# Kernel tuning notes

Measured on AMD Instinct MI355X. Metric: run time of the kernel, lower is better.

The kernel has to match this reference:

```python
import jax, jax.numpy as jnp
import numpy as np

TOP_K = 2
NUM_EXPERTS = 8


def setup_inputs() -> dict:
    key = jax.random.key(0)
    ks = jax.random.split(key, 8)
    h, d, ds, E = 1024, 512, 1024, NUM_EXPERTS
    s = 1.0 / np.sqrt(h)
    return {
        "x": jax.random.normal(ks[0], (2, 2048, h), jnp.float32),
        "router": jax.random.normal(ks[1], (h, E), jnp.float32) * s,
        "experts_gate": jax.random.normal(ks[2], (E, h, d), jnp.float32) * s,
        "experts_up": jax.random.normal(ks[3], (E, h, d), jnp.float32) * s,
        "experts_down": jax.random.normal(ks[4], (E, d, h), jnp.float32) * (1.0 / np.sqrt(d)),
        "shared_gate": jax.random.normal(ks[5], (h, ds), jnp.float32) * s,
        "shared_up": jax.random.normal(ks[6], (h, ds), jnp.float32) * s,
        "shared_down": jax.random.normal(ks[7], (ds, h), jnp.float32) * (1.0 / np.sqrt(ds)),
    }


def reference(x, router, experts_gate, experts_up, experts_down,
              shared_gate, shared_up, shared_down):
    b, s, h = x.shape
    E = router.shape[1]
    # Shared expert path (SwiGLU)
    shared_act = jax.nn.silu(jnp.einsum('bsh,hd->bsd', x, shared_gate))
    shared_up_out = jnp.einsum('bsh,hd->bsd', x, shared_up)
    shared_out = jnp.einsum('bsd,dh->bsh', shared_act * shared_up_out, shared_down)
    # Router: softmax over experts, top-k selection
    router_probs = jax.nn.softmax(jnp.einsum('bsh,he->bse', x, router), axis=-1)
    topk_probs, topk_idx = jax.lax.top_k(router_probs, TOP_K)  # [b,s,k]
    # Dense per-token expert coefficient matrix: coef[t,e] = prob if expert e selected else 0
    coef = jnp.sum(jax.nn.one_hot(topk_idx, E, dtype=x.dtype) * topk_probs[..., None], axis=2)
    coef = coef.reshape(b * s, E)  # [T,E]
    x_flat = x.reshape(b * s, h)
    # Grouped expert SwiGLU (mathematically identical to gather->gemm->scatter_add;
    # unrouted token contributions are zeroed by coef)
    gate = jnp.einsum('th,ehd->etd', x_flat, experts_gate)
    up = jnp.einsum('th,ehd->etd', x_flat, experts_up)
    expert_out = jnp.einsum('etd,edh->eth', jax.nn.silu(gate) * up, experts_down)
    routed = jnp.einsum('eth,te->th', expert_out, coef)
    return routed.reshape(b, s, h) + shared_out
```

## Files before the change

kernel.cpp:

```cpp
#include <hip/hip_runtime.h>
#include <hip/hip_bf16.h>
#include <stdint.h>

typedef short bf16x8 __attribute__((ext_vector_type(8)));
typedef float f32x4 __attribute__((ext_vector_type(4)));
typedef unsigned short u16;

#define GLOAD16(gp, lp)                                                        \
  __builtin_amdgcn_global_load_lds(                                            \
      (const __attribute__((address_space(1))) void*)(gp),                     \
      (__attribute__((address_space(3))) void*)(lp), 16, 0, 0)

__device__ __forceinline__ u16 f2bf(float f) {
  uint32_t u = __builtin_bit_cast(uint32_t, f);
  u = (u + 0x7FFFu + ((u >> 16) & 1u)) >> 16;
  return (u16)u;
}
__device__ __forceinline__ float bf2f(u16 v) {
  return __builtin_bit_cast(float, (uint32_t)v << 16);
}

__device__ __forceinline__ int swzoff(int row, int u) {
  int p = row >> 1;
  int us = ((row & 1) * 4 + u) ^ (p & 7);
  return p * 128 + us * 16;
}

__global__ void mega(const float* __restrict__ x, const float* __restrict__ rw,
                     const float* __restrict__ eg, const float* __restrict__ eu,
                     const float* __restrict__ ed, const float* __restrict__ sg,
                     const float* __restrict__ su, const float* __restrict__ sd,
                     u16* __restrict__ Xb, u16* __restrict__ WpT,
                     u16* __restrict__ Wd2, u16* __restrict__ Wds,
                     float4* __restrict__ meta) {
  __shared__ float t[64][65];
  const int tid = threadIdx.x;
  const int b = blockIdx.x;
  if (b < 1280) {
    const float* src; int k0, h0;
    const bool is_e = b < 1024;
    if (is_e) { src = ed; k0 = (b >> 4) * 64;          h0 = (b & 15) * 64; }
    else      { src = sd; k0 = ((b - 1024) >> 4) * 64; h0 = (b & 15) * 64; }
#pragma unroll
    for (int p = 0; p < 4; ++p) {
      int r = p * 16 + (tid >> 4), c = (tid & 15) * 4;
      float4 v = *(const float4*)&src[(size_t)(k0 + r) * 1024 + h0 + c];
      t[r][c] = v.x; t[r][c + 1] = v.y; t[r][c + 2] = v.z; t[r][c + 3] = v.w;
    }
    __syncthreads();
#pragma unroll
    for (int p = 0; p < 4; ++p) {
      int hl = p * 16 + (tid >> 4), kl = (tid & 15) * 4;
      ushort4 o;
      o.x = f2bf(t[kl][hl]);     o.y = f2bf(t[kl + 1][hl]);
      o.z = f2bf(t[kl + 2][hl]); o.w = f2bf(t[kl + 3][hl]);
      if (is_e) {
        int kk = k0 + kl;
        int e = kk >> 9, dk = kk & 511;
        *(ushort4*)&Wd2[(size_t)e * 524288 + (size_t)(h0 + hl) * 512 + dk] = o;
      } else {
        *(ushort4*)&Wds[(size_t)(h0 + hl) * 1024 + k0 + kl] = o;
      }
    }
  } else if (b < 3840) {
    int bb = b - 1280;
    const float* src; int pbase, C, dt, ht;
    if (bb < 2048) {
      int slice = bb >> 7, r = bb & 127;
      int e = slice >> 1; int up = slice & 1;
      src = (up ? eu : eg) + (size_t)e * 524288;
      pbase = e * 1024 + up * 32; C = 512;
      dt = r >> 4; ht = r & 15;
    } else {
      int r = bb - 2048;
      int up = r >= 256; r &= 255;
      src = up ? su : sg; pbase = 8192 + up * 32; C = 1024;
      dt = r >> 4; ht = r & 15;
    }
    const int d0 = dt * 64, h0 = ht * 64;
#pragma unroll
    for (int p = 0; p < 4; ++p) {
      int hl = p * 16 + (tid >> 4), dl = (tid & 15) * 4;
      float4 v = *(const float4*)&src[(size_t)(h0 + hl) * C + d0 + dl];
      t[hl][dl] = v.x; t[hl][dl + 1] = v.y; t[hl][dl + 2] = v.z; t[hl][dl + 3] = v.w;
    }
    __syncthreads();
#pragma unroll
    for (int p = 0; p < 4; ++p) {
      int dl = p * 16 + (tid >> 4), hl = (tid & 15) * 4;
      int d = d0 + dl;
      int prow = pbase + ((d >> 5) << 6) + (d & 31);
      ushort4 o;
      o.x = f2bf(t[hl][dl]);     o.y = f2bf(t[hl + 1][dl]);
      o.z = f2bf(t[hl + 2][dl]); o.w = f2bf(t[hl + 3][dl]);
      *(ushort4*)&WpT[(size_t)prow * 1024 + h0 + hl] = o;
    }
  } else if (b < 4864) {
    const int l = tid & 63;
    const int tok = (b - 3840) * 4 + (tid >> 6);
    const float* xr = x + (size_t)tok * 1024;
    float acc[8];
#pragma unroll
    for (int e = 0; e < 8; ++e) acc[e] = 0.f;
    for (int it = 0; it < 16; ++it) {
      int h = it * 64 + l;
      float xv = xr[h];
      float4 r0 = *(const float4*)&rw[h * 8];
      float4 r1 = *(const float4*)&rw[h * 8 + 4];
      acc[0] += xv * r0.x; acc[1] += xv * r0.y; acc[2] += xv * r0.z; acc[3] += xv * r0.w;
      acc[4] += xv * r1.x; acc[5] += xv * r1.y; acc[6] += xv * r1.z; acc[7] += xv * r1.w;
    }
#pragma unroll
    for (int off = 32; off >= 1; off >>= 1) {
#pragma unroll
      for (int e = 0; e < 8; ++e) acc[e] += __shfl_xor(acc[e], off, 64);
    }
    if (l == 0) {
      float m = acc[0];
#pragma unroll
      for (int e = 1; e < 8; ++e) m = fmaxf(m, acc[e]);
      float p[8], s = 0.f;
#pragma unroll
      for (int e = 0; e < 8; ++e) { p[e] = expf(acc[e] - m); s += p[e]; }
      int i1 = 0;
#pragma unroll
      for (int e = 1; e < 8; ++e) if (p[e] > p[i1]) i1 = e;
      int i2 = (i1 == 0) ? 1 : 0;
#pragma unroll
      for (int e = 0; e < 8; ++e) if (e != i1 && p[e] > p[i2]) i2 = e;
      float inv = 1.f / s;
      meta[tok] = make_float4(__int_as_float(i1), __int_as_float(i2),
                              p[i1] * inv, p[i2] * inv);
    }
  } else {
    int i = (b - 4864) * 512 + tid;
#pragma unroll
    for (int k = 0; k < 2; ++k) {
      float4 v = ((const float4*)x)[i + k * 256];
      ushort4 o;
      o.x = f2bf(v.x); o.y = f2bf(v.y); o.z = f2bf(v.z); o.w = f2bf(v.w);
      ((ushort4*)Xb)[i + k * 256] = o;
    }
  }
}

__global__ __launch_bounds__(512) void assign_k(const float4* __restrict__ meta,
                                                int* __restrict__ counts_g,
                                                int* __restrict__ list_tok,
                                                int2* __restrict__ t2s) {
  __shared__ u16 sel[4096];
  __shared__ int cnt_s[8];
  const int tid = threadIdx.x;
  for (int i = tid; i < 4096; i += 512) {
    float4 m = meta[i];
    sel[i] = (u16)(__float_as_int(m.x) | (__float_as_int(m.y) << 8));
  }
  __syncthreads();

  const int E = tid >> 6;
  const int lane = tid & 63;
  const unsigned long long lt = (lane == 63) ? ~0ull >> 1 : ((1ull << lane) - 1ull);

  int total = 0;
#pragma unroll 8
  for (int it = 0; it < 64; ++it) {
    u16 s = sel[it * 64 + lane];
    bool any = ((s & 255) == E) || ((s >> 8) == E);
    total += __popcll(__ballot(any));
  }
  if (lane == 0) { cnt_s[E] = total; counts_g[E] = total; }
  __syncthreads();
  int base = 0;
#pragma unroll
  for (int e = 0; e < 8; ++e) base += (e < E) ? cnt_s[e] : 0;

  int running = base;
  for (int it = 0; it < 64; ++it) {
    int tok = it * 64 + lane;
    u16 s = sel[tok];
    bool s1 = ((s & 255) == E);
    bool s2 = ((s >> 8) == E);
    unsigned long long mask = __ballot(s1 || s2);
    int pos = running + __popcll(mask & lt);
    if (s1 || s2) {
      list_tok[pos] = tok;
      if (s1) t2s[tok].x = pos;
      else    t2s[tok].y = pos;
    }
    running += __popcll(mask);
  }
}

template <int MODE>
__global__ __launch_bounds__(512, 2) void moe_gemm(
    const u16* __restrict__ Xb, const u16* __restrict__ WpT,
    const u16* __restrict__ Wd2, const u16* __restrict__ Wds,
    u16* __restrict__ Hs, u16* __restrict__ Hcomp, u16* __restrict__ Pb,
    u16* __restrict__ Ps0, u16* __restrict__ Ps1,
    const int* __restrict__ counts, const int* __restrict__ list_tok) {
  constexpr int SLOT = (128 + 256) * 64;
  constexpr int BOFF = 128 * 64;
  __shared__ __align__(16) char lds[3 * SLOT];

  const int tid = threadIdx.x;
  const int l = tid & 63, l15 = l & 15, lg = l >> 4;
  const int wv = tid >> 6, wr = wv >> 2, wc = wv & 3;

  const int id = blockIdx.x;
  const bool routed = id < 288;
  int expert = 0, m0 = 0, n0 = 0, base = 0, count = 0, nt, split = 0, kb = 0;

  if (routed) {
    int mtf = id >> 2; n0 = (id & 3) * 256;
    int acc_ = 0, bas = 0, found = 0;
#pragma unroll
    for (int e = 0; e < 8; ++e) {
      int c = counts[e];
      int nm = (c + 127) >> 7;
      if (!found && mtf < acc_ + nm) {
        expert = e; m0 = (mtf - acc_) * 128; base = bas; count = c; found = 1;
      }
      acc_ += nm; bas += c;
    }
    if (!found) return;
  } else {
    int sid = id - 288;
    int xcd = sid & 7, pos = sid >> 3;
    int mG = xcd >> 1, nG = xcd & 1;
    if (MODE == 0) {
      int mL = pos & 7, nL = pos >> 3;
      m0 = (mG * 8 + mL) * 128; n0 = (nG * 4 + nL) * 256;
    } else {
      split = pos & 1;
      int q = pos >> 1;
      int mL = q & 7, nL = q >> 3;
      m0 = (mG * 8 + mL) * 128; n0 = (nG * 2 + nL) * 256;
      kb = split * 512;
    }
  }
  nt = (MODE == 1) ? 16 : 32;

  const char* gA0; const char* gB[2]; int lA0, lB[2];
  {
    int L = tid * 16;
    int p = L >> 7, uph = (L >> 4) & 7;
    int usw = uph ^ (p & 7);
    int row = 2 * p + (usw >> 2), ulog = usw & 3;
    const u16* ap;
    if (MODE == 0) {
      if (routed) {
        int ar = min(m0 + row, count - 1);
        ap = Xb + (size_t)list_tok[base + ar] * 1024;
      } else ap = Xb + (size_t)(m0 + row) * 1024;
    } else {
      if (routed) ap = Hcomp + (size_t)(base + min(m0 + row, count - 1)) * 512;
      else        ap = Hs + (size_t)(m0 + row) * 1024 + kb;
    }
    gA0 = (const char*)ap + ulog * 16;
    lA0 = L;
  }
#pragma unroll
  for (int j = 0; j < 2; ++j) {
    int L = (j * 512 + tid) * 16;
    int p = L >> 7, uph = (L >> 4) & 7;
    int usw = uph ^ (p & 7);
    int row = 2 * p + (usw >> 2), ulog = usw & 3;
    const u16* bp;
    if (MODE == 0) {
      int rbase = routed ? expert * 1024 : 8192;
      bp = WpT + (size_t)(rbase + n0 + row) * 1024;
    } else {
      if (routed) bp = Wd2 + (size_t)expert * 524288 + (size_t)(n0 + row) * 512;
      else        bp = Wds + (size_t)(n0 + row) * 1024 + kb;
    }
    gB[j] = (const char*)bp + ulog * 16;
    lB[j] = L;
  }

  int offA[4], offB[4];
#pragma unroll
  for (int m = 0; m < 4; ++m) offA[m] = swzoff(wr * 64 + m * 16 + l15, lg);
#pragma unroll
  for (int n = 0; n < 4; ++n) offB[n] = BOFF + swzoff(wc * 64 + n * 16 + l15, lg);

  f32x4 acc[4][4];
#pragma unroll
  for (int m = 0; m < 4; ++m)
#pragma unroll
    for (int n = 0; n < 4; ++n) acc[m][n] = {0.f, 0.f, 0.f, 0.f};

#define STAGE(T)                                                               \
  {                                                                            \
    char* sb_ = lds + (((T) % 3) * SLOT);                                      \
    const int tb_ = (T) * 64;                                                  \
    GLOAD16(gA0 + tb_, sb_ + lA0);                                             \
    GLOAD16(gB[0] + tb_, sb_ + BOFF + lB[0]);                                  \
    GLOAD16(gB[1] + tb_, sb_ + BOFF + lB[1]);                                  \
  }

  STAGE(0); STAGE(1);

  for (int t = 0; t < nt; ++t) {
    if (t + 1 < nt) {
      asm volatile("s_waitcnt vmcnt(3)" ::: "memory");
    } else {
      asm volatile("s_waitcnt vmcnt(0)" ::: "memory");
    }
    __builtin_amdgcn_s_barrier();
    asm volatile("" ::: "memory");
    char* sb = lds + ((t % 3) * SLOT);
    bf16x8 af[4], bfr[4];
#pragma unroll
    for (int m = 0; m < 4; ++m) af[m] = *(const bf16x8*)(sb + offA[m]);
#pragma unroll
    for (int n = 0; n < 4; ++n) bfr[n] = *(const bf16x8*)(sb + offB[n]);
    if (t + 2 < nt) STAGE(t + 2);
    __builtin_amdgcn_s_setprio(1);
#pragma unroll
    for (int m = 0; m < 4; ++m)
#pragma unroll
      for (int n = 0; n < 4; ++n)
        acc[m][n] = __builtin_amdgcn_mfma_f32_16x16x32_bf16(af[m], bfr[n], acc[m][n], 0, 0, 0);
    __builtin_amdgcn_s_setprio(0);
    asm volatile("" ::: "memory");
  }
#undef STAGE

  const int rbl = wr * 64 + lg * 4;
  const int cnt_lim = routed ? count : (1 << 30);
  if constexpr (MODE == 0) {
    u16* dst = routed ? Hcomp : Hs;
    const int ldH = routed ? 512 : 1024;
    const int rowbase = routed ? (base + m0) : m0;
    const int cD0 = (n0 + wc * 64) >> 1;
#pragma unroll
    for (int m = 0; m < 4; ++m)
#pragma unroll
      for (int q = 0; q < 2; ++q) {
        int cD = cD0 + q * 16 + l15;
#pragma unroll
        for (int j = 0; j < 4; ++j) {
          int mrow = rbl + m * 16 + j;
          if (m0 + mrow < cnt_lim) {
            float g = acc[m][q][j];
            float u = acc[m][q + 2][j];
            dst[(size_t)(rowbase + mrow) * ldH + cD] =
                f2bf(g / (1.f + __expf(-g)) * u);
          }
        }
      }
  } else {
    const int cb = n0 + wc * 64;
    u16* dstS = split ? Ps1 : Ps0;
#pragma unroll
    for (int m = 0; m < 4; ++m)
#pragma unroll
      for (int n = 0; n < 4; ++n)
#pragma unroll
        for (int j = 0; j < 4; ++j) {
          int mrow = rbl + m * 16 + j;
          if (m0 + mrow < cnt_lim) {
            int col = cb + n * 16 + l15;
            if (routed)
              Pb[(size_t)(base + m0 + mrow) * 1024 + col] = f2bf(acc[m][n][j]);
            else
              dstS[(size_t)(m0 + mrow) * 1024 + col] = f2bf(acc[m][n][j]);
          }
        }
  }
}

__global__ void reduce_k(const float4* __restrict__ meta, const int2* __restrict__ t2s,
                         const u16* __restrict__ Pb, const u16* __restrict__ Ps0,
                         const u16* __restrict__ Ps1, float* __restrict__ out) {
  const int t = blockIdx.x;
  const int c = threadIdx.x * 4;
  float4 m = meta[t];
  int2 s = t2s[t];
  float p1 = m.z, p2 = m.w;
  ushort4 a  = *(const ushort4*)&Pb[(size_t)s.x * 1024 + c];
  ushort4 bb = *(const ushort4*)&Pb[(size_t)s.y * 1024 + c];
  ushort4 u0 = *(const ushort4*)&Ps0[(size_t)t * 1024 + c];
  ushort4 u1 = *(const ushort4*)&Ps1[(size_t)t * 1024 + c];
  float4 o;
  o.x = bf2f(u0.x) + bf2f(u1.x) + p1 * bf2f(a.x) + p2 * bf2f(bb.x);
  o.y = bf2f(u0.y) + bf2f(u1.y) + p1 * bf2f(a.y) + p2 * bf2f(bb.y);
  o.z = bf2f(u0.z) + bf2f(u1.z) + p1 * bf2f(a.z) + p2 * bf2f(bb.z);
  o.w = bf2f(u0.w) + bf2f(u1.w) + p1 * bf2f(a.w) + p2 * bf2f(bb.w);
  *(float4*)&out[(size_t)t * 1024 + c] = o;
}

extern "C" void kernel_launch(void* const* d_in, const int* in_sizes, int n_in,
                              void* d_out, int out_size, void* d_ws, size_t ws_size,
                              hipStream_t stream) {
  const float* x  = (const float*)d_in[0];
  const float* rw = (const float*)d_in[1];
  const float* eg = (const float*)d_in[2];
  const float* eu = (const float*)d_in[3];
  const float* ed = (const float*)d_in[4];
  const float* sg = (const float*)d_in[5];
  const float* su = (const float*)d_in[6];
  const float* sd = (const float*)d_in[7];
  float* out = (float*)d_out;

  char* ws = (char*)d_ws;
  u16*    Xb    = (u16*)(ws);
  u16*    WpT   = (u16*)(ws + 8388608);
  u16*    Ps0   = (u16*)(ws + 8388608);
  u16*    Ps1   = (u16*)(ws + 16777216);
  u16*    Wd2   = (u16*)(ws + 29360128);
  u16*    Wds   = (u16*)(ws + 37748736);
  u16*    Hs    = (u16*)(ws + 39845888);
  u16*    Hcomp = (u16*)(ws + 48234496);
  u16*    Pb    = (u16*)(ws + 56623104);
  float4* meta  = (float4*)(ws + 73400320);
  int2*   t2s   = (int2*)(ws + 73465856);
  int*    counts= (int*)(ws + 73498624);
  int*    list_tok = (int*)(ws + 73498688);

  mega<<<6912, 256, 0, stream>>>(x, rw, eg, eu, ed, sg, su, sd,
                                 Xb, WpT, Wd2, Wds, meta);
  assign_k<<<1, 512, 0, stream>>>(meta, counts, list_tok, t2s);

  moe_gemm<0><<<544, 512, 0, stream>>>(Xb, WpT, Wd2, Wds, Hs, Hcomp, Pb,
                                       Ps0, Ps1, counts, list_tok);
  moe_gemm<1><<<544, 512, 0, stream>>>(Xb, WpT, Wd2, Wds, Hs, Hcomp, Pb,
                                       Ps0, Ps1, counts, list_tok);

  reduce_k<<<4096, 256, 0, stream>>>(meta, t2s, Pb, Ps0, Ps1, out);
}
```

Before: 125.9 us.

## Double-buffer MFMA fragments in registers and deepen global-to-LDS prefetch

Restructures the GEMM main loop into a two-step unrolled pipeline. LDS-to-register fragment loads for the next k-tile are issued before the MFMAs of the current tile, using ping-pong register sets, and global-to-LDS staging runs three tiles ahead instead of two. The aim is to hide LDS read latency and global load latency behind matrix-core work. In exchange it uses more VGPRs, which can lower occupancy. It also assumes the tile count is even, and the three-slot LDS ring now depends on tighter barrier and waitcnt ordering.

```diff
diff --git a/kernel.cpp b/kernel.cpp
--- a/kernel.cpp
+++ b/kernel.cpp
@@ -297,34 +297,53 @@
     GLOAD16(gB[0] + tb_, sb_ + BOFF + lB[0]);                                  \
     GLOAD16(gB[1] + tb_, sb_ + BOFF + lB[1]);                                  \
   }
-
-  STAGE(0); STAGE(1);
-
-  for (int t = 0; t < nt; ++t) {
-    if (t + 1 < nt) {
-      asm volatile("s_waitcnt vmcnt(3)" ::: "memory");
-    } else {
-      asm volatile("s_waitcnt vmcnt(0)" ::: "memory");
-    }
-    __builtin_amdgcn_s_barrier();
-    asm volatile("" ::: "memory");
-    char* sb = lds + ((t % 3) * SLOT);
-    bf16x8 af[4], bfr[4];
-#pragma unroll
-    for (int m = 0; m < 4; ++m) af[m] = *(const bf16x8*)(sb + offA[m]);
-#pragma unroll
-    for (int n = 0; n < 4; ++n) bfr[n] = *(const bf16x8*)(sb + offB[n]);
-    if (t + 2 < nt) STAGE(t + 2);
-    __builtin_amdgcn_s_setprio(1);
-#pragma unroll
-    for (int m = 0; m < 4; ++m)
-#pragma unroll
-      for (int n = 0; n < 4; ++n)
-        acc[m][n] = __builtin_amdgcn_mfma_f32_16x16x32_bf16(af[m], bfr[n], acc[m][n], 0, 0, 0);
-    __builtin_amdgcn_s_setprio(0);
-    asm volatile("" ::: "memory");
+#define LOADFRAG(AF, BF, T)                                                    \
+  {                                                                            \
+    char* sb_ = lds + (((T) % 3) * SLOT);                                      \
+    _Pragma("unroll") for (int q = 0; q < 4; ++q) {                            \
+      AF[q] = *(const bf16x8*)(sb_ + offA[q]);                                 \
+      BF[q] = *(const bf16x8*)(sb_ + offB[q]);                                 \
+    }                                                                          \
+  }
+#define MMAC(AF, BF)                                                           \
+  {                                                                            \
+    __builtin_amdgcn_s_setprio(1);                                             \
+    _Pragma("unroll") for (int m = 0; m < 4; ++m)                              \
+        _Pragma("unroll") for (int n = 0; n < 4; ++n)                          \
+            acc[m][n] = __builtin_amdgcn_mfma_f32_16x16x32_bf16(               \
+                AF[m], BF[n], acc[m][n], 0, 0, 0);                             \
+    __builtin_amdgcn_s_setprio(0);                                             \
+  }
+#define ENDSTEP(COND3)                                                         \
+  {                                                                            \
+    if (COND3) asm volatile("s_waitcnt vmcnt(3) lgkmcnt(0)" ::: "memory");     \
+    else       asm volatile("s_waitcnt vmcnt(0) lgkmcnt(0)" ::: "memory");     \
+    __builtin_amdgcn_s_barrier();                                              \
+  }
+
+  bf16x8 aE[4], bE[4], aO[4], bO[4];
+
+  STAGE(0); STAGE(1); STAGE(2);
+  asm volatile("s_waitcnt vmcnt(6)" ::: "memory");
+  __builtin_amdgcn_s_barrier();
+  LOADFRAG(aE, bE, 0);
+  asm volatile("s_waitcnt vmcnt(3) lgkmcnt(0)" ::: "memory");
+  __builtin_amdgcn_s_barrier();
+
+  for (int t = 0; t < nt; t += 2) {
+    LOADFRAG(aO, bO, t + 1);
+    if (t + 3 < nt) STAGE(t + 3);
+    MMAC(aE, bE);
+    ENDSTEP(t + 3 < nt);
+    if (t + 2 < nt) LOADFRAG(aE, bE, t + 2);
+    if (t + 4 < nt) STAGE(t + 4);
+    MMAC(aO, bO);
+    ENDSTEP(t + 4 < nt);
   }
 #undef STAGE
+#undef LOADFRAG
+#undef MMAC
+#undef ENDSTEP
 
   const int rbl = wr * 64 + lg * 4;
   const int cnt_lim = routed ? count : (1 << 30);
```

Measured after the change: 136.3 us. 1.08x slower.
